# Performance work log

Hardware: AMD Instinct MI355X
Metric: run time of the kernel (lower is better)

## Reference

```python
import jax, jax.numpy as jnp
import numpy as np
import math

B, S, D, H, HD, P = 2, 2048, 2048, 16, 128, 10
ROPE_BASE = 10000.0


def _rope_tables(seq_len, head_dim):
    inv_freq = 1.0 / (ROPE_BASE ** (np.arange(0, head_dim, 2, dtype=np.float32) / head_dim))
    t = np.arange(seq_len, dtype=np.float32)
    freqs = np.outer(t, inv_freq)                  # [S, hd/2]
    emb = np.concatenate([freqs, freqs], axis=-1)  # [S, hd]
    return jnp.asarray(np.cos(emb)), jnp.asarray(np.sin(emb))


def _rotate_half(x):
    half = x.shape[-1] // 2
    return jnp.concatenate([-x[..., half:], x[..., :half]], axis=-1)


def setup_inputs() -> dict:
    key = jax.random.key(0)
    ks = jax.random.split(key, 8)
    hidden_states = jax.random.normal(ks[0], (B, S, D), dtype=jnp.float32)
    # causal additive mask, llama convention: 0 where allowed, large negative above diagonal
    causal = jnp.triu(jnp.full((S, S), -1e9, dtype=jnp.float32), k=1)
    attention_mask = jnp.broadcast_to(causal[None, None], (B, 1, S, S))
    position_ids = jnp.broadcast_to(jnp.arange(S, dtype=jnp.int64)[None], (B, S))
    scale = 1.0 / math.sqrt(D)
    Wq = jax.random.normal(ks[1], (D, D), dtype=jnp.float32) * scale
    Wk = jax.random.normal(ks[2], (D, D), dtype=jnp.float32) * scale
    Wv = jax.random.normal(ks[3], (D, D), dtype=jnp.float32) * scale
    Wo = jax.random.normal(ks[4], (D, D), dtype=jnp.float32) * scale
    adapter_query = jax.random.normal(ks[5], (P, D), dtype=jnp.float32)
    adapter_gate = jax.random.normal(ks[6], (1, H, 1, 1), dtype=jnp.float32) * 0.1
    return dict(hidden_states=hidden_states, attention_mask=attention_mask,
                position_ids=position_ids, Wq=Wq, Wk=Wk, Wv=Wv, Wo=Wo,
                adapter_query=adapter_query, adapter_gate=adapter_gate)


def reference(hidden_states, attention_mask, position_ids, Wq, Wk, Wv, Wo,
              adapter_query, adapter_gate):
    bsz, q_len, _ = hidden_states.shape
    inv_sqrt_hd = 1.0 / math.sqrt(HD)

    def split_heads(x):  # [B,S,D] -> [B,H,S,hd]
        return x.reshape(bsz, q_len, H, HD).transpose(0, 2, 1, 3)

    q = split_heads(hidden_states @ Wq)
    k = split_heads(hidden_states @ Wk)
    v = split_heads(hidden_states @ Wv)

    # RoPE
    cos_t, sin_t = _rope_tables(q_len, HD)
    cos = cos_t[position_ids][:, None]  # [B,1,S,hd]
    sin = sin_t[position_ids][:, None]
    q = q * cos + _rotate_half(q) * sin
    k = k * cos + _rotate_half(k) * sin

    # main attention
    scores = jnp.einsum('bhqd,bhkd->bhqk', q, k) * inv_sqrt_hd
    scores = scores + attention_mask
    attn = jax.nn.softmax(scores.astype(jnp.float32), axis=-1).astype(q.dtype)
    attn_out = jnp.einsum('bhqk,bhkd->bhqd', attn, v)

    # adapter: soft prompt projected through k/v proj (learn_kv=False), no RoPE
    adapter = jnp.broadcast_to(adapter_query[None], (bsz, P, D))  # [B,P,D]
    a_k = (adapter @ Wk).reshape(bsz, P, H, HD).transpose(0, 2, 1, 3)  # [B,H,P,hd]
    a_v = (adapter @ Wv).reshape(bsz, P, H, HD).transpose(0, 2, 1, 3)
    a_scores = jnp.einsum('bhqd,bhpd->bhqp', q, a_k) * inv_sqrt_hd
    a_w = adapter_gate * jax.nn.softmax(a_scores.astype(jnp.float32), axis=-1).astype(q.dtype)
    a_out = jnp.einsum('bhqp,bhpd->bhqd', a_w, a_v)

    out = attn_out + a_out
    out = out.transpose(0, 2, 1, 3).reshape(bsz, q_len, D)
    return out @ Wo
```

## Files before the change

kernel.cpp:

```cpp
#include <hip/hip_runtime.h>
#include <cstdint>
#include <cstddef>

typedef __bf16 bf16x8 __attribute__((ext_vector_type(8)));
typedef float  f32x4  __attribute__((ext_vector_type(4)));

__device__ __forceinline__ unsigned short f2bf(float f) {
  unsigned int u = __float_as_uint(f);
  u += 0x7FFF + ((u >> 16) & 1);
  return (unsigned short)(u >> 16);
}
__device__ __forceinline__ float bf2f(unsigned short u) {
  return __uint_as_float(((unsigned int)u) << 16);
}

#define SEQ 2048
#define DMODEL 2048
#define NH 16
#define HD 128
#define NB 2
#define NP 10
#define MAUG 4106
#define SCALEL2 (0.08838834764831845f * 1.44269504088896340f)

#define GLOAD_LDS16(g, l) \
  __builtin_amdgcn_global_load_lds((__attribute__((address_space(1))) const void*)(g), \
                                   (__attribute__((address_space(3))) void*)(l), 16, 0, 0)

#define FENCE() asm volatile("" ::: "memory")
#define SBAR() do { FENCE(); __builtin_amdgcn_s_barrier(); FENCE(); } while (0)
#define WAITVM(N) asm volatile("s_waitcnt vmcnt(" #N ")" ::: "memory")

__global__ void k_tables(float* __restrict__ cost, float* __restrict__ sint) {
  int idx = blockIdx.x * 256 + threadIdx.x;
  if (idx >= SEQ * 64) return;
  int s = idx >> 6, i = idx & 63;
  double invf = exp(-((double)(2 * i) / 128.0) * log(10000.0));
  double a = (double)s * invf;
  float c = (float)cos(a), sn = (float)sin(a);
  cost[s * HD + i] = c;  cost[s * HD + 64 + i] = c;
  sint[s * HD + i] = sn; sint[s * HD + 64 + i] = sn;
}

__global__ __launch_bounds__(256) void k_wt(const float* __restrict__ W0,
                                            const float* __restrict__ W1,
                                            const float* __restrict__ W2,
                                            const float* __restrict__ W3,
                                            unsigned short* __restrict__ out) {
  __shared__ float tile[32][33];
  const float* W = (blockIdx.z == 0) ? W0 : (blockIdx.z == 1) ? W1 : (blockIdx.z == 2) ? W2 : W3;
  unsigned short* o = out + (size_t)blockIdx.z * DMODEL * DMODEL;
  int bx = blockIdx.x * 32, by = blockIdx.y * 32;
  int tx = threadIdx.x & 31, ty = threadIdx.x >> 5;
  #pragma unroll
  for (int j = 0; j < 32; j += 8)
    tile[ty + j][tx] = W[(size_t)(bx + ty + j) * DMODEL + by + tx];
  __syncthreads();
  #pragma unroll
  for (int j = 0; j < 32; j += 8)
    o[(size_t)(by + ty + j) * DMODEL + bx + tx] = f2bf(tile[tx][ty + j]);
}

__global__ void k_xaug(const float* __restrict__ X, const float* __restrict__ Aq,
                       unsigned short* __restrict__ xaug) {
  size_t idx = (size_t)blockIdx.x * 256 + threadIdx.x;
  if (idx >= (size_t)MAUG * DMODEL) return;
  size_t row = idx >> 11;
  int col = (int)(idx & 2047);
  float v = (row < (size_t)NB * SEQ) ? X[idx] : Aq[(row - NB * SEQ) * DMODEL + col];
  xaug[idx] = f2bf(v);
}

#define LDA_HALF(MH) do { \
  _Pragma("unroll") for (int i_ = 0; i_ < 4; i_++) \
    _Pragma("unroll") for (int ks_ = 0; ks_ < 2; ks_++) \
      a[i_][ks_] = *(const bf16x8*)&lds[base + (wr*128 + (MH)*64 + i_*16 + lr)*64 + (((ks_*4+quad) ^ (lr & 7)) * 8)]; \
} while (0)

#define LDB_PAIR(NH) do { \
  _Pragma("unroll") for (int j_ = 0; j_ < 2; j_++) \
    _Pragma("unroll") for (int ks_ = 0; ks_ < 2; ks_++) \
      b[(NH)*2+j_][ks_] = *(const bf16x8*)&lds[base + 16384 + (wc*64 + ((NH)*2+j_)*16 + lr)*64 + (((ks_*4+quad) ^ (lr & 7)) * 8)]; \
} while (0)

#define MFMA_QUAD(MH, NH) do { \
  __builtin_amdgcn_s_setprio(1); \
  _Pragma("unroll") for (int i_ = 0; i_ < 4; i_++) \
    _Pragma("unroll") for (int j_ = 0; j_ < 2; j_++) { \
      acc[(MH)*4+i_][(NH)*2+j_] = __builtin_amdgcn_mfma_f32_16x16x32_bf16(a[i_][0], b[(NH)*2+j_][0], acc[(MH)*4+i_][(NH)*2+j_], 0, 0, 0); \
      acc[(MH)*4+i_][(NH)*2+j_] = __builtin_amdgcn_mfma_f32_16x16x32_bf16(a[i_][1], b[(NH)*2+j_][1], acc[(MH)*4+i_][(NH)*2+j_], 0, 0, 0); \
    } \
  __builtin_amdgcn_s_setprio(0); \
} while (0)

#define STG_AE(nb, ko) do { \
  GLOAD_LDS16(sA + (ko),                      &lds[(nb)*32768 + (qrow)*64 + g8]); \
  GLOAD_LDS16(sA + 128*(size_t)DMODEL + (ko), &lds[(nb)*32768 + (128+qrow)*64 + g8]); } while (0)
#define STG_AO(nb, ko) do { \
  GLOAD_LDS16(sA + 64*(size_t)DMODEL + (ko),  &lds[(nb)*32768 + (64+qrow)*64 + g8]); \
  GLOAD_LDS16(sA + 192*(size_t)DMODEL + (ko), &lds[(nb)*32768 + (192+qrow)*64 + g8]); } while (0)
#define STG_BE(nb, ko) do { \
  GLOAD_LDS16(sB + (ko),                      &lds[(nb)*32768 + 16384 + (qb)*64 + g8]); \
  GLOAD_LDS16(sB + 128*(size_t)DMODEL + (ko), &lds[(nb)*32768 + 16384 + (128+qb)*64 + g8]); } while (0)
#define STG_BO(nb, ko) do { \
  GLOAD_LDS16(sB + 32*(size_t)DMODEL + (ko),  &lds[(nb)*32768 + 16384 + (32+qb)*64 + g8]); \
  GLOAD_LDS16(sB + 160*(size_t)DMODEL + (ko), &lds[(nb)*32768 + 16384 + (160+qb)*64 + g8]); } while (0)

template<int BF16OUT>
__global__ __launch_bounds__(512, 2) void k_gemm256(const unsigned short* __restrict__ A,
                                                    const unsigned short* __restrict__ Bt,
                                                    void* __restrict__ Cv,
                                                    int M, size_t c_stride_mat) {
  __shared__ unsigned short lds[65536];
  const int t = threadIdx.x;
  const int lane = t & 63, w = t >> 6;
  const int lr = lane & 15, quad = lane >> 4;
  const int wr = w >> 2, wc = w & 3;
  const int m0 = blockIdx.y * 256, n0 = blockIdx.x * 256;
  const unsigned short* Bz = Bt + (size_t)blockIdx.z * DMODEL * DMODEL;

  const int qrow = t >> 3;
  const int g8 = (t & 7) * 8;
  const int gsw8 = (((t & 7) ^ (qrow & 7)) * 8);
  const int qb = (qrow < 32) ? qrow : qrow + 32;

  const unsigned short* sA = A + (size_t)(m0 + qrow) * DMODEL + gsw8;
  const unsigned short* sB = Bz + (size_t)(n0 + qb) * DMODEL + gsw8;

  bf16x8 a[4][2], b[4][2];
  f32x4 acc[8][4];
  #pragma unroll
  for (int i = 0; i < 8; i++)
    #pragma unroll
    for (int j = 0; j < 4; j++) acc[i][j] = (f32x4){0.f, 0.f, 0.f, 0.f};

  STG_AE(0, 0); STG_BE(0, 0); STG_BO(0, 0); STG_AO(0, 0);
  WAITVM(4);
  SBAR();

  for (int kt = 0; kt < DMODEL / 64; kt++) {
    const int base = (kt & 1) << 15;
    const int nb = (kt & 1) ^ 1;
    const int ko = (kt + 1) * 64;
    const bool more = (kt + 1 < DMODEL / 64);

    LDA_HALF(0);
    LDB_PAIR(0);
    if (more) STG_AE(nb, ko);
    SBAR();
    MFMA_QUAD(0, 0);
    if (more) WAITVM(4); else WAITVM(2);
    SBAR();

    LDB_PAIR(1);
    if (more) STG_BE(nb, ko);
    SBAR();
    MFMA_QUAD(0, 1);
    if (more) WAITVM(4); else WAITVM(0);
    SBAR();

    LDA_HALF(1);
    if (more) STG_BO(nb, ko);
    SBAR();
    MFMA_QUAD(1, 0);
    SBAR();

    if (more) STG_AO(nb, ko);
    SBAR();
    MFMA_QUAD(1, 1);
    if (more) WAITVM(4);
    SBAR();
  }

  #pragma unroll
  for (int mi = 0; mi < 8; mi++) {
    #pragma unroll
    for (int r = 0; r < 4; r++) {
      int row = m0 + wr * 128 + mi * 16 + quad * 4 + r;
      if (row < M) {
        if (BF16OUT) {
          unsigned short* C = (unsigned short*)Cv + (size_t)blockIdx.z * c_stride_mat;
          #pragma unroll
          for (int n = 0; n < 4; n++)
            C[(size_t)row * DMODEL + n0 + wc * 64 + n * 16 + lr] = f2bf(acc[mi][n][r]);
        } else {
          float* C = (float*)Cv + (size_t)blockIdx.z * c_stride_mat;
          #pragma unroll
          for (int n = 0; n < 4; n++)
            C[(size_t)row * DMODEL + n0 + wc * 64 + n * 16 + lr] = acc[mi][n][r];
        }
      }
    }
  }
}

__global__ __launch_bounds__(256) void k_rope(const unsigned short* __restrict__ Qf,
                                              const unsigned short* __restrict__ Kf,
                                              const unsigned short* __restrict__ Vf,
                                              const float* __restrict__ cost, const float* __restrict__ sint,
                                              unsigned short* __restrict__ Qb, unsigned short* __restrict__ Kb,
                                              unsigned short* __restrict__ AKb, unsigned short* __restrict__ avt) {
  int row = blockIdx.x;
  int t = threadIdx.x;
  int c0 = t * 8;
  size_t off = (size_t)row * DMODEL + c0;
  if (row < NB * SEQ) {
    int s = row & (SEQ - 1);
    int d0 = c0 & (HD - 1);
    int po = (d0 < 64) ? 64 : -64;
    float sign = (d0 < 64) ? -1.f : 1.f;
    uint4 qv = *(const uint4*)&Qf[off];
    uint4 qp = *(const uint4*)&Qf[off + po];
    uint4 kv = *(const uint4*)&Kf[off];
    uint4 kp = *(const uint4*)&Kf[off + po];
    const unsigned short* qa = (const unsigned short*)&qv;
    const unsigned short* qb2 = (const unsigned short*)&qp;
    const unsigned short* ka = (const unsigned short*)&kv;
    const unsigned short* kb2 = (const unsigned short*)&kp;
    unsigned short oq[8], ok[8];
    #pragma unroll
    for (int j = 0; j < 8; j++) {
      float cv = cost[s * HD + d0 + j], sv = sint[s * HD + d0 + j];
      oq[j] = f2bf(bf2f(qa[j]) * cv + sign * bf2f(qb2[j]) * sv);
      ok[j] = f2bf(bf2f(ka[j]) * cv + sign * bf2f(kb2[j]) * sv);
    }
    *(uint4*)&Qb[off] = *(const uint4*)oq;
    *(uint4*)&Kb[off] = *(const uint4*)ok;
  } else {
    int p = row - NB * SEQ;
    uint4 kv = *(const uint4*)&Kf[off];
    uint4 vv = *(const uint4*)&Vf[off];
    *(uint4*)&AKb[(size_t)p * DMODEL + c0] = kv;
    const unsigned short* vp = (const unsigned short*)&vv;
    #pragma unroll
    for (int j = 0; j < 8; j++)
      avt[(size_t)(c0 + j) * 32 + p] = vp[j];
  }
}

__global__ __launch_bounds__(256) void k_vt(const unsigned short* __restrict__ Vf,
                                            unsigned short* __restrict__ Vt) {
  __shared__ unsigned short tile[64][72];
  const int t = threadIdx.x;
  int s0 = blockIdx.x * 64;
  int d0 = blockIdx.y * 64;
  int b = blockIdx.z >> 4, h = blockIdx.z & 15;
  #pragma unroll
  for (int j = t; j < 512; j += 256) {
    int row = j >> 3, ch = j & 7;
    *(uint4*)&tile[row][ch * 8] =
      *(const uint4*)&Vf[(size_t)(b * SEQ + s0 + row) * DMODEL + h * HD + d0 + ch * 8];
  }
  __syncthreads();
  #pragma unroll
  for (int j = t; j < 512; j += 256) {
    int dr = j >> 3, ch = j & 7;
    unsigned short tmp[8];
    #pragma unroll
    for (int k = 0; k < 8; k++) tmp[k] = tile[ch * 8 + k][dr];
    *(uint4*)&Vt[((size_t)((b * NH + h) * HD + d0 + dr)) * SEQ + s0 + ch * 8] = *(const uint4*)tmp;
  }
}

#define PSTR 68

__global__ __launch_bounds__(256, 3) void k_flash(const unsigned short* __restrict__ Qb,
                                               const unsigned short* __restrict__ Kb,
                                               const unsigned short* __restrict__ Vt,
                                               const unsigned short* __restrict__ AKb,
                                               const unsigned short* __restrict__ avt,
                                               const float* __restrict__ gate,
                                               unsigned short* __restrict__ Obuf,
                                               float* __restrict__ ml,
                                               unsigned short* __restrict__ Aout) {
  const int L = blockIdx.x;
  const int h = L & 15;
  const int slot = 39 - (L >> 4);
  const int b = blockIdx.y;
  int qt, j, P;
  if (slot < 4)       { qt = slot;               j = 0;          P = 1; }
  else if (slot < 12) { int s = slot - 4;  qt = 4 + (s >> 1);  j = s & 1; P = 2; }
  else if (slot < 24) { int s = slot - 12; qt = 8 + s / 3;     j = s % 3; P = 3; }
  else                { int s = slot - 24; qt = 12 + (s >> 2); j = s & 3; P = 4; }

  const int t = threadIdx.x, w = t >> 6, lane = t & 63;
  const int lr = lane & 15, quad = lane >> 4;

  __shared__ unsigned short Ks[64 * 128];
  __shared__ unsigned short Vs[128 * 64];
  __shared__ unsigned short Ps[4][32 * PSTR];
  unsigned short* Ps16 = &Ps[w][0];

  const int row_base = qt * 128 + w * 32;

  bf16x8 qf[2][4];
  #pragma unroll
  for (int mt = 0; mt < 2; mt++)
    #pragma unroll
    for (int kk = 0; kk < 4; kk++)
      qf[mt][kk] = *(const bf16x8*)&Qb[((size_t)(b * SEQ + row_base + mt * 16 + lr)) * DMODEL
                                       + h * HD + kk * 32 + quad * 8];

  f32x4 o[2][8];
  #pragma unroll
  for (int mt = 0; mt < 2; mt++)
    #pragma unroll
    for (int nt = 0; nt < 8; nt++) o[mt][nt] = (f32x4){0.f, 0.f, 0.f, 0.f};
  float l_i[2][4];
  #pragma unroll
  for (int mt = 0; mt < 2; mt++)
    #pragma unroll
    for (int r = 0; r < 4; r++) l_i[mt][r] = 0.f;

  const int krow = t >> 4;
  const int vd = t >> 3, vc = (t & 7) ^ (vd & 7);
  const int ktend = 2 * qt + 2;

  for (int kt = j; kt < ktend; kt += P) {
    __syncthreads();
    #pragma unroll
    for (int jj = 0; jj < 4; jj++) {
      int row = krow + jj * 16;
      int c = (t & 15) ^ (row & 15);
      GLOAD_LDS16(&Kb[((size_t)(b * SEQ + kt * 64 + row)) * DMODEL + h * HD + c * 8],
                  &Ks[(t + jj * 256) * 8]);
    }
    #pragma unroll
    for (int jj = 0; jj < 4; jj++) {
      int d = vd + jj * 32;
      GLOAD_LDS16(&Vt[((size_t)((b * NH + h) * HD + d)) * SEQ + kt * 64 + vc * 8],
                  &Vs[(t + jj * 256) * 8]);
    }
    __syncthreads();

    f32x4 s4[2][4];
    #pragma unroll
    for (int mt = 0; mt < 2; mt++)
      #pragma unroll
      for (int nt = 0; nt < 4; nt++) s4[mt][nt] = (f32x4){0.f, 0.f, 0.f, 0.f};
    #pragma unroll
    for (int nt = 0; nt < 4; nt++)
      #pragma unroll
      for (int kk = 0; kk < 4; kk++) {
        bf16x8 bv = *(const bf16x8*)&Ks[((nt * 16 + lr) * 16 + ((kk * 4 + quad) ^ lr)) * 8];
        s4[0][nt] = __builtin_amdgcn_mfma_f32_16x16x32_bf16(qf[0][kk], bv, s4[0][nt], 0, 0, 0);
        s4[1][nt] = __builtin_amdgcn_mfma_f32_16x16x32_bf16(qf[1][kk], bv, s4[1][nt], 0, 0, 0);
      }

    const int maybe_mask = (kt * 64 + 63 > row_base);
    #pragma unroll
    for (int mt = 0; mt < 2; mt++) {
      #pragma unroll
      for (int nt = 0; nt < 4; nt++) s4[mt][nt] = s4[mt][nt] * SCALEL2;
      if (maybe_mask) {
        #pragma unroll
        for (int nt = 0; nt < 4; nt++) {
          int col = kt * 64 + nt * 16 + lr;
          #pragma unroll
          for (int r = 0; r < 4; r++)
            if (col > row_base + mt * 16 + quad * 4 + r) s4[mt][nt][r] = -__builtin_inff();
        }
      }
      #pragma unroll
      for (int nt = 0; nt < 4; nt++)
        #pragma unroll
        for (int r = 0; r < 4; r++) {
          float p = __builtin_amdgcn_exp2f(s4[mt][nt][r]);
          l_i[mt][r] += p;
          Ps[w][(mt * 16 + quad * 4 + r) * PSTR + nt * 16 + lr] = f2bf(p);
        }
    }
    #pragma unroll
    for (int kk2 = 0; kk2 < 2; kk2++) {
      bf16x8 af0 = *(const bf16x8*)&Ps[w][(lr) * PSTR + kk2 * 32 + quad * 8];
      bf16x8 af1 = *(const bf16x8*)&Ps[w][(16 + lr) * PSTR + kk2 * 32 + quad * 8];
      #pragma unroll
      for (int nt = 0; nt < 8; nt++) {
        bf16x8 bv = *(const bf16x8*)&Vs[((nt * 16 + lr) * 8 + ((kk2 * 4 + quad) ^ (lr & 7))) * 8];
        o[0][nt] = __builtin_amdgcn_mfma_f32_16x16x32_bf16(af0, bv, o[0][nt], 0, 0, 0);
        o[1][nt] = __builtin_amdgcn_mfma_f32_16x16x32_bf16(af1, bv, o[1][nt], 0, 0, 0);
      }
    }
  }

  #pragma unroll
  for (int mt = 0; mt < 2; mt++)
    #pragma unroll
    for (int r = 0; r < 4; r++) {
      float l = l_i[mt][r];
      #pragma unroll
      for (int off = 1; off < 16; off <<= 1) l += __shfl_xor(l, off, 64);
      l_i[mt][r] = l;
    }

  const size_t slotg = (size_t)(b * 16 + h) * 40 + slot;

  if (j == 0) {
    const float g = gate[h];
    #pragma unroll
    for (int mt = 0; mt < 2; mt++) {
      f32x4 as4 = (f32x4){0.f, 0.f, 0.f, 0.f};
      #pragma unroll
      for (int kk = 0; kk < 4; kk++) {
        bf16x8 akf = *(const bf16x8*)&AKb[(size_t)lr * DMODEL + h * HD + kk * 32 + quad * 8];
        as4 = __builtin_amdgcn_mfma_f32_16x16x32_bf16(qf[mt][kk], akf, as4, 0, 0, 0);
      }
      as4 = as4 * SCALEL2;
      float al[4];
      #pragma unroll
      for (int r = 0; r < 4; r++) {
        float p = (lr < NP) ? __builtin_amdgcn_exp2f(as4[r]) : 0.f;
        as4[r] = p;
        float sum = p;
        #pragma unroll
        for (int off = 1; off < 16; off <<= 1) sum += __shfl_xor(sum, off, 64);
        al[r] = sum;
      }
      #pragma unroll
      for (int r = 0; r < 4; r++) {
        Ps[w][(mt * 16 + quad * 4 + r) * PSTR + lr] = f2bf(as4[r]);
        Ps[w][(mt * 16 + quad * 4 + r) * PSTR + 16 + lr] = 0;
      }
      bf16x8 af = *(const bf16x8*)&Ps[w][(mt * 16 + lr) * PSTR + quad * 8];
      f32x4 pa[8];
      #pragma unroll
      for (int nt = 0; nt < 8; nt++) {
        bf16x8 bv = *(const bf16x8*)&avt[(size_t)(h * HD + nt * 16 + lr) * 32 + quad * 8];
        pa[nt] = __builtin_amdgcn_mfma_f32_16x16x32_bf16(af, bv, (f32x4){0.f, 0.f, 0.f, 0.f}, 0, 0, 0);
      }
      float invla[4];
      #pragma unroll
      for (int r = 0; r < 4; r++) invla[r] = g / al[r];
      #pragma unroll
      for (int nt = 0; nt < 8; nt++)
        #pragma unroll
        for (int r = 0; r < 4; r++)
          Ps16[(quad * 4 + r) * 128 + nt * 16 + lr] = f2bf(pa[nt][r] * invla[r]);
      size_t gb = (((size_t)(b * 16 + h) * 16 + qt)) * 16384 + (size_t)(w * 32 + mt * 16) * 128;
      #pragma unroll
      for (int it = 0; it < 4; it++) {
        int i = lane + it * 64;
        int rr = i >> 4, ch = i & 15;
        *(uint4*)&Aout[gb + rr * 128 + ch * 8] = *(const uint4*)&Ps16[rr * 128 + ch * 8];
      }
    }
  }

  #pragma unroll
  for (int mt = 0; mt < 2; mt++) {
    if (lr == 0) {
      #pragma unroll
      for (int r = 0; r < 4; r++) {
        int rl = w * 32 + mt * 16 + quad * 4 + r;
        ml[slotg * 128 + rl] = l_i[mt][r];
      }
    }
    #pragma unroll
    for (int nt = 0; nt < 8; nt++)
      #pragma unroll
      for (int r = 0; r < 4; r++)
        Ps16[(quad * 4 + r) * 128 + nt * 16 + lr] = f2bf(o[mt][nt][r]);
    size_t gb = slotg * 16384 + (size_t)(w * 32 + mt * 16) * 128;
    #pragma unroll
    for (int it = 0; it < 4; it++) {
      int i = lane + it * 64;
      int rr = i >> 4, ch = i & 15;
      *(uint4*)&Obuf[gb + rr * 128 + ch * 8] = *(const uint4*)&Ps16[rr * 128 + ch * 8];
    }
  }
}

__global__ __launch_bounds__(256) void k_merge(const unsigned short* __restrict__ Obuf,
                                               const float* __restrict__ ml,
                                               const unsigned short* __restrict__ Aout,
                                               unsigned short* __restrict__ ab) {
  int idx = blockIdx.x * 256 + threadIdx.x;
  int ch = idx & 15;
  int row = (idx >> 4) & 2047;
  int h = (idx >> 15) & 15;
  int b = idx >> 19;
  int qt = row >> 7, rl = row & 127;
  int start = qt < 4 ? qt : qt < 8 ? 4 + 2 * (qt - 4) : qt < 12 ? 12 + 3 * (qt - 8) : 24 + 4 * (qt - 12);
  int P = qt < 4 ? 1 : qt < 8 ? 2 : qt < 12 ? 3 : 4;
  size_t sbase = (size_t)(b * 16 + h) * 40 + start;
  float den = 0.f;
  float acc[8] = {0.f, 0.f, 0.f, 0.f, 0.f, 0.f, 0.f, 0.f};
  #pragma unroll
  for (int jp = 0; jp < 4; jp++) {
    if (jp < P) {
      den += ml[(sbase + jp) * 128 + rl];
      uint4 ov = *(const uint4*)&Obuf[(sbase + jp) * 16384 + rl * 128 + ch * 8];
      const unsigned short* pv = (const unsigned short*)&ov;
      #pragma unroll
      for (int k = 0; k < 8; k++) acc[k] += bf2f(pv[k]);
    }
  }
  uint4 av = *(const uint4*)&Aout[(((size_t)(b * 16 + h) * 16 + qt)) * 16384 + rl * 128 + ch * 8];
  const unsigned short* pa = (const unsigned short*)&av;
  float dn = 1.0f / den;
  unsigned short res[8];
  #pragma unroll
  for (int k = 0; k < 8; k++) res[k] = f2bf(acc[k] * dn + bf2f(pa[k]));
  *(uint4*)&ab[((size_t)(b * 2048 + row)) * 2048 + h * 128 + ch * 8] = *(const uint4*)res;
}

extern "C" void kernel_launch(void* const* d_in, const int* in_sizes, int n_in,
                              void* d_out, int out_size, void* d_ws, size_t ws_size,
                              hipStream_t stream) {
  const float* hidden = (const float*)d_in[0];
  const float* Wq = (const float*)d_in[3];
  const float* Wk = (const float*)d_in[4];
  const float* Wv = (const float*)d_in[5];
  const float* Wo = (const float*)d_in[6];
  const float* Aq = (const float*)d_in[7];
  const float* gate = (const float*)d_in[8];
  float* out = (float*)d_out;

  char* ws = (char*)d_ws;
  size_t off = 0;
  auto alloc = [&](size_t bytes) -> void* {
    void* p = ws + off;
    off = (off + bytes + 255) & ~(size_t)255;
    return p;
  };
  unsigned short* wt   = (unsigned short*)alloc((size_t)4 * DMODEL * DMODEL * 2);
  unsigned short* xaug = (unsigned short*)alloc((size_t)MAUG * DMODEL * 2);
  unsigned short* qkvb = (unsigned short*)alloc((size_t)3 * MAUG * DMODEL * 2);
  unsigned short* qf = qkvb;
  unsigned short* kf = qkvb + (size_t)MAUG * DMODEL;
  unsigned short* vf = kf + (size_t)MAUG * DMODEL;
  unsigned short* qb  = (unsigned short*)alloc((size_t)NB * SEQ * DMODEL * 2);
  unsigned short* kb  = (unsigned short*)alloc((size_t)NB * SEQ * DMODEL * 2);
  unsigned short* vt  = (unsigned short*)alloc((size_t)NB * SEQ * DMODEL * 2);
  unsigned short* akb = (unsigned short*)alloc((size_t)16 * DMODEL * 2);
  unsigned short* avt = (unsigned short*)alloc((size_t)DMODEL * 32 * 2);
  float* cost = (float*)alloc((size_t)SEQ * HD * 4);
  float* sint = (float*)alloc((size_t)SEQ * HD * 4);
  unsigned short* obuf = (unsigned short*)alloc((size_t)NB * NH * 40 * 16384 * 2);
  float* mlb = (float*)alloc((size_t)NB * NH * 40 * 128 * 4);
  unsigned short* aout = (unsigned short*)alloc((size_t)NB * NH * 16 * 16384 * 2);
  unsigned short* ab = qf;

  k_tables<<<SEQ * 64 / 256, 256, 0, stream>>>(cost, sint);
  k_wt<<<dim3(64, 64, 4), 256, 0, stream>>>(Wq, Wk, Wv, Wo, wt);
  {
    size_t n = (size_t)MAUG * DMODEL;
    k_xaug<<<(unsigned)((n + 255) / 256), 256, 0, stream>>>(hidden, Aq, xaug);
  }
  k_gemm256<1><<<dim3(8, 17, 3), 512, 0, stream>>>(xaug, wt, qkvb, MAUG, (size_t)MAUG * DMODEL);
  hipMemsetAsync(avt, 0, (size_t)DMODEL * 32 * 2, stream);
  k_rope<<<MAUG, 256, 0, stream>>>(qf, kf, vf, cost, sint, qb, kb, akb, avt);
  k_vt<<<dim3(32, 2, 32), 256, 0, stream>>>(vf, vt);
  k_flash<<<dim3(640, 2), 256, 0, stream>>>(qb, kb, vt, akb, avt, gate, obuf, mlb, aout);
  k_merge<<<4096, 256, 0, stream>>>(obuf, mlb, aout, ab);
  k_gemm256<0><<<dim3(8, 16, 1), 512, 0, stream>>>(ab, wt + (size_t)3 * DMODEL * DMODEL, out, NB * SEQ, 0);
}
```

Baseline: 481.6 us.

## Add 128x256 tile output-projection GEMM with two blocks per CU and lgkm waits

```diff
diff --git a/kernel.cpp b/kernel.cpp
--- a/kernel.cpp
+++ b/kernel.cpp
@@ -30,6 +30,7 @@
 #define FENCE() asm volatile("" ::: "memory")
 #define SBAR() do { FENCE(); __builtin_amdgcn_s_barrier(); FENCE(); } while (0)
 #define WAITVM(N) asm volatile("s_waitcnt vmcnt(" #N ")" ::: "memory")
+#define HINTLGKM(N) asm volatile("s_waitcnt lgkmcnt(" #N ")" ::: "memory")
 
 __global__ void k_tables(float* __restrict__ cost, float* __restrict__ sint) {
   int idx = blockIdx.x * 256 + threadIdx.x;
@@ -77,18 +78,18 @@
       a[i_][ks_] = *(const bf16x8*)&lds[base + (wr*128 + (MH)*64 + i_*16 + lr)*64 + (((ks_*4+quad) ^ (lr & 7)) * 8)]; \
 } while (0)
 
-#define LDB_PAIR(NH) do { \
+#define LDB_PAIR(NHH) do { \
   _Pragma("unroll") for (int j_ = 0; j_ < 2; j_++) \
     _Pragma("unroll") for (int ks_ = 0; ks_ < 2; ks_++) \
-      b[(NH)*2+j_][ks_] = *(const bf16x8*)&lds[base + 16384 + (wc*64 + ((NH)*2+j_)*16 + lr)*64 + (((ks_*4+quad) ^ (lr & 7)) * 8)]; \
+      b[(NHH)*2+j_][ks_] = *(const bf16x8*)&lds[base + 16384 + (wc*64 + ((NHH)*2+j_)*16 + lr)*64 + (((ks_*4+quad) ^ (lr & 7)) * 8)]; \
 } while (0)
 
-#define MFMA_QUAD(MH, NH) do { \
+#define MFMA_QUAD(MH, NHH) do { \
   __builtin_amdgcn_s_setprio(1); \
   _Pragma("unroll") for (int i_ = 0; i_ < 4; i_++) \
     _Pragma("unroll") for (int j_ = 0; j_ < 2; j_++) { \
-      acc[(MH)*4+i_][(NH)*2+j_] = __builtin_amdgcn_mfma_f32_16x16x32_bf16(a[i_][0], b[(NH)*2+j_][0], acc[(MH)*4+i_][(NH)*2+j_], 0, 0, 0); \
-      acc[(MH)*4+i_][(NH)*2+j_] = __builtin_amdgcn_mfma_f32_16x16x32_bf16(a[i_][1], b[(NH)*2+j_][1], acc[(MH)*4+i_][(NH)*2+j_], 0, 0, 0); \
+      acc[(MH)*4+i_][(NHH)*2+j_] = __builtin_amdgcn_mfma_f32_16x16x32_bf16(a[i_][0], b[(NHH)*2+j_][0], acc[(MH)*4+i_][(NHH)*2+j_], 0, 0, 0); \
+      acc[(MH)*4+i_][(NHH)*2+j_] = __builtin_amdgcn_mfma_f32_16x16x32_bf16(a[i_][1], b[(NHH)*2+j_][1], acc[(MH)*4+i_][(NHH)*2+j_], 0, 0, 0); \
     } \
   __builtin_amdgcn_s_setprio(0); \
 } while (0)
@@ -147,6 +148,7 @@
     LDA_HALF(0);
     LDB_PAIR(0);
     if (more) STG_AE(nb, ko);
+    HINTLGKM(8);
     SBAR();
     MFMA_QUAD(0, 0);
     if (more) WAITVM(4); else WAITVM(2);
@@ -161,6 +163,7 @@
 
     LDA_HALF(1);
     if (more) STG_BO(nb, ko);
+    HINTLGKM(4);
     SBAR();
     MFMA_QUAD(1, 0);
     SBAR();
@@ -190,6 +193,113 @@
             C[(size_t)row * DMODEL + n0 + wc * 64 + n * 16 + lr] = acc[mi][n][r];
         }
       }
+    }
+  }
+}
+
+#define O_LDA(MH) do { \
+  _Pragma("unroll") for (int i_ = 0; i_ < 2; i_++) \
+    _Pragma("unroll") for (int ks_ = 0; ks_ < 2; ks_++) \
+      a[i_][ks_] = *(const bf16x8*)&lds[base + (wr*64 + ((MH)*2+i_)*16 + lr)*64 + (((ks_*4+quad) ^ (lr & 7)) * 8)]; \
+} while (0)
+
+#define O_LDB(NHH) do { \
+  _Pragma("unroll") for (int j_ = 0; j_ < 2; j_++) \
+    _Pragma("unroll") for (int ks_ = 0; ks_ < 2; ks_++) \
+      b[(NHH)*2+j_][ks_] = *(const bf16x8*)&lds[base + 8192 + (wc*64 + ((NHH)*2+j_)*16 + lr)*64 + (((ks_*4+quad) ^ (lr & 7)) * 8)]; \
+} while (0)
+
+#define O_MFMA(MH, NHH) do { \
+  __builtin_amdgcn_s_setprio(1); \
+  _Pragma("unroll") for (int i_ = 0; i_ < 2; i_++) \
+    _Pragma("unroll") for (int j_ = 0; j_ < 2; j_++) { \
+      acc[(MH)*2+i_][(NHH)*2+j_] = __builtin_amdgcn_mfma_f32_16x16x32_bf16(a[i_][0], b[(NHH)*2+j_][0], acc[(MH)*2+i_][(NHH)*2+j_], 0, 0, 0); \
+      acc[(MH)*2+i_][(NHH)*2+j_] = __builtin_amdgcn_mfma_f32_16x16x32_bf16(a[i_][1], b[(NHH)*2+j_][1], acc[(MH)*2+i_][(NHH)*2+j_], 0, 0, 0); \
+    } \
+  __builtin_amdgcn_s_setprio(0); \
+} while (0)
+
+#define O_STG_AE(nb, ko) GLOAD_LDS16(sA + (ko), &lds[(nb)*24576 + (qb)*64 + g8])
+#define O_STG_AO(nb, ko) GLOAD_LDS16(sA + 32*(size_t)DMODEL + (ko), &lds[(nb)*24576 + (32+qb)*64 + g8])
+#define O_STG_BE(nb, ko) do { \
+  GLOAD_LDS16(sB + (ko),                      &lds[(nb)*24576 + 8192 + (qb)*64 + g8]); \
+  GLOAD_LDS16(sB + 128*(size_t)DMODEL + (ko), &lds[(nb)*24576 + 8192 + (128+qb)*64 + g8]); } while (0)
+#define O_STG_BO(nb, ko) do { \
+  GLOAD_LDS16(sB + 32*(size_t)DMODEL + (ko),  &lds[(nb)*24576 + 8192 + (32+qb)*64 + g8]); \
+  GLOAD_LDS16(sB + 160*(size_t)DMODEL + (ko), &lds[(nb)*24576 + 8192 + (160+qb)*64 + g8]); } while (0)
+
+__global__ __launch_bounds__(512, 2) void k_gemmo(const unsigned short* __restrict__ A,
+                                                  const unsigned short* __restrict__ Bt,
+                                                  float* __restrict__ C) {
+  __shared__ unsigned short lds[49152];
+  const int t = threadIdx.x;
+  const int lane = t & 63, w = t >> 6;
+  const int lr = lane & 15, quad = lane >> 4;
+  const int wr = w >> 2, wc = w & 3;
+  const int m0 = blockIdx.y * 128, n0 = blockIdx.x * 256;
+
+  const int qrow = t >> 3;
+  const int g8 = (t & 7) * 8;
+  const int gsw8 = (((t & 7) ^ (qrow & 7)) * 8);
+  const int qb = (qrow < 32) ? qrow : qrow + 32;
+
+  const unsigned short* sA = A + (size_t)(m0 + qb) * DMODEL + gsw8;
+  const unsigned short* sB = Bt + (size_t)(n0 + qb) * DMODEL + gsw8;
+
+  bf16x8 a[2][2], b[4][2];
+  f32x4 acc[4][4];
+  #pragma unroll
+  for (int i = 0; i < 4; i++)
+    #pragma unroll
+    for (int j = 0; j < 4; j++) acc[i][j] = (f32x4){0.f, 0.f, 0.f, 0.f};
+
+  O_STG_AE(0, 0); O_STG_BE(0, 0); O_STG_BO(0, 0); O_STG_AO(0, 0);
+  WAITVM(3);
+  SBAR();
+
+  for (int kt = 0; kt < DMODEL / 64; kt++) {
+    const int base = (kt & 1) * 24576;
+    const int nb = (kt & 1) ^ 1;
+    const int ko = (kt + 1) * 64;
+    const bool more = (kt + 1 < DMODEL / 64);
+
+    O_LDA(0);
+    O_LDB(0);
+    if (more) O_STG_AE(nb, ko);
+    HINTLGKM(4);
+    SBAR();
+    O_MFMA(0, 0);
+    if (more) WAITVM(2); else WAITVM(1);
+    SBAR();
+
+    O_LDB(1);
+    if (more) O_STG_BE(nb, ko);
+    SBAR();
+    O_MFMA(0, 1);
+    if (more) WAITVM(3); else WAITVM(0);
+    SBAR();
+
+    O_LDA(1);
+    if (more) O_STG_BO(nb, ko);
+    SBAR();
+    O_MFMA(1, 0);
+    SBAR();
+
+    if (more) O_STG_AO(nb, ko);
+    SBAR();
+    O_MFMA(1, 1);
+    if (more) WAITVM(3);
+    SBAR();
+  }
+
+  #pragma unroll
+  for (int mi = 0; mi < 4; mi++) {
+    #pragma unroll
+    for (int r = 0; r < 4; r++) {
+      int row = m0 + wr * 64 + mi * 16 + quad * 4 + r;
+      #pragma unroll
+      for (int n = 0; n < 4; n++)
+        C[(size_t)row * DMODEL + n0 + wc * 64 + n * 16 + lr] = acc[mi][n][r];
     }
   }
 }
@@ -553,5 +663,5 @@
   k_vt<<<dim3(32, 2, 32), 256, 0, stream>>>(vf, vt);
   k_flash<<<dim3(640, 2), 256, 0, stream>>>(qb, kb, vt, akb, avt, gate, obuf, mlb, aout);
   k_merge<<<4096, 256, 0, stream>>>(obuf, mlb, aout, ab);
-  k_gemm256<0><<<dim3(8, 16, 1), 512, 0, stream>>>(ab, wt + (size_t)3 * DMODEL * DMODEL, out, NB * SEQ, 0);
-}
+  k_gemmo<<<dim3(8, 32), 512, 0, stream>>>(ab, wt + (size_t)3 * DMODEL * DMODEL, out);
+}
```

Measured after the change: 471.9 us. 1.02x faster.

## Shrink GEMM tiles to 128x128 with register double-buffering and XCD-aware block mapping

Applied to the files above, without the earlier changes.

```diff
diff --git a/kernel.cpp b/kernel.cpp
--- a/kernel.cpp
+++ b/kernel.cpp
@@ -71,120 +71,121 @@
   xaug[idx] = f2bf(v);
 }
 
-#define LDA_HALF(MH) do { \
-  _Pragma("unroll") for (int i_ = 0; i_ < 4; i_++) \
+#define RD_A(dst, bb, MH) do { \
+  _Pragma("unroll") for (int i_ = 0; i_ < 2; i_++) \
     _Pragma("unroll") for (int ks_ = 0; ks_ < 2; ks_++) \
-      a[i_][ks_] = *(const bf16x8*)&lds[base + (wr*128 + (MH)*64 + i_*16 + lr)*64 + (((ks_*4+quad) ^ (lr & 7)) * 8)]; \
+      dst[i_][ks_] = *(const bf16x8*)&lds[(bb) + (wr*64 + (MH)*32 + i_*16 + lr)*64 + (((ks_*4+quad) ^ (lr & 7)) * 8)]; \
 } while (0)
 
-#define LDB_PAIR(NH) do { \
+#define RD_B(dst, bb, NHH) do { \
   _Pragma("unroll") for (int j_ = 0; j_ < 2; j_++) \
     _Pragma("unroll") for (int ks_ = 0; ks_ < 2; ks_++) \
-      b[(NH)*2+j_][ks_] = *(const bf16x8*)&lds[base + 16384 + (wc*64 + ((NH)*2+j_)*16 + lr)*64 + (((ks_*4+quad) ^ (lr & 7)) * 8)]; \
+      dst[j_][ks_] = *(const bf16x8*)&lds[(bb) + 8192 + (wc*64 + (NHH)*32 + j_*16 + lr)*64 + (((ks_*4+quad) ^ (lr & 7)) * 8)]; \
 } while (0)
 
-#define MFMA_QUAD(MH, NH) do { \
+#define MM(A, B, MH, NHH) do { \
   __builtin_amdgcn_s_setprio(1); \
-  _Pragma("unroll") for (int i_ = 0; i_ < 4; i_++) \
+  _Pragma("unroll") for (int i_ = 0; i_ < 2; i_++) \
     _Pragma("unroll") for (int j_ = 0; j_ < 2; j_++) { \
-      acc[(MH)*4+i_][(NH)*2+j_] = __builtin_amdgcn_mfma_f32_16x16x32_bf16(a[i_][0], b[(NH)*2+j_][0], acc[(MH)*4+i_][(NH)*2+j_], 0, 0, 0); \
-      acc[(MH)*4+i_][(NH)*2+j_] = __builtin_amdgcn_mfma_f32_16x16x32_bf16(a[i_][1], b[(NH)*2+j_][1], acc[(MH)*4+i_][(NH)*2+j_], 0, 0, 0); \
+      acc[(MH)*2+i_][(NHH)*2+j_] = __builtin_amdgcn_mfma_f32_16x16x32_bf16(A[i_][0], B[j_][0], acc[(MH)*2+i_][(NHH)*2+j_], 0, 0, 0); \
+      acc[(MH)*2+i_][(NHH)*2+j_] = __builtin_amdgcn_mfma_f32_16x16x32_bf16(A[i_][1], B[j_][1], acc[(MH)*2+i_][(NHH)*2+j_], 0, 0, 0); \
     } \
   __builtin_amdgcn_s_setprio(0); \
 } while (0)
 
 #define STG_AE(nb, ko) do { \
-  GLOAD_LDS16(sA + (ko),                      &lds[(nb)*32768 + (qrow)*64 + g8]); \
-  GLOAD_LDS16(sA + 128*(size_t)DMODEL + (ko), &lds[(nb)*32768 + (128+qrow)*64 + g8]); } while (0)
+  GLOAD_LDS16(sA + (ko),                     &lds[(nb)*16384 + (qrow)*64 + g8]); \
+  GLOAD_LDS16(sA + 64*(size_t)DMODEL + (ko), &lds[(nb)*16384 + (64+qrow)*64 + g8]); } while (0)
 #define STG_AO(nb, ko) do { \
-  GLOAD_LDS16(sA + 64*(size_t)DMODEL + (ko),  &lds[(nb)*32768 + (64+qrow)*64 + g8]); \
-  GLOAD_LDS16(sA + 192*(size_t)DMODEL + (ko), &lds[(nb)*32768 + (192+qrow)*64 + g8]); } while (0)
+  GLOAD_LDS16(sA + 32*(size_t)DMODEL + (ko), &lds[(nb)*16384 + (32+qrow)*64 + g8]); \
+  GLOAD_LDS16(sA + 96*(size_t)DMODEL + (ko), &lds[(nb)*16384 + (96+qrow)*64 + g8]); } while (0)
 #define STG_BE(nb, ko) do { \
-  GLOAD_LDS16(sB + (ko),                      &lds[(nb)*32768 + 16384 + (qb)*64 + g8]); \
-  GLOAD_LDS16(sB + 128*(size_t)DMODEL + (ko), &lds[(nb)*32768 + 16384 + (128+qb)*64 + g8]); } while (0)
+  GLOAD_LDS16(sB + (ko),                     &lds[(nb)*16384 + 8192 + (qrow)*64 + g8]); \
+  GLOAD_LDS16(sB + 64*(size_t)DMODEL + (ko), &lds[(nb)*16384 + 8192 + (64+qrow)*64 + g8]); } while (0)
 #define STG_BO(nb, ko) do { \
-  GLOAD_LDS16(sB + 32*(size_t)DMODEL + (ko),  &lds[(nb)*32768 + 16384 + (32+qb)*64 + g8]); \
-  GLOAD_LDS16(sB + 160*(size_t)DMODEL + (ko), &lds[(nb)*32768 + 16384 + (160+qb)*64 + g8]); } while (0)
+  GLOAD_LDS16(sB + 32*(size_t)DMODEL + (ko), &lds[(nb)*16384 + 8192 + (32+qrow)*64 + g8]); \
+  GLOAD_LDS16(sB + 96*(size_t)DMODEL + (ko), &lds[(nb)*16384 + 8192 + (96+qrow)*64 + g8]); } while (0)
 
 template<int BF16OUT>
-__global__ __launch_bounds__(512, 2) void k_gemm256(const unsigned short* __restrict__ A,
+__global__ __launch_bounds__(256, 2) void k_gemm128(const unsigned short* __restrict__ A,
                                                     const unsigned short* __restrict__ Bt,
                                                     void* __restrict__ Cv,
                                                     int M, size_t c_stride_mat) {
-  __shared__ unsigned short lds[65536];
+  __shared__ unsigned short lds[32768];
   const int t = threadIdx.x;
   const int lane = t & 63, w = t >> 6;
   const int lr = lane & 15, quad = lane >> 4;
-  const int wr = w >> 2, wc = w & 3;
-  const int m0 = blockIdx.y * 256, n0 = blockIdx.x * 256;
-  const unsigned short* Bz = Bt + (size_t)blockIdx.z * DMODEL * DMODEL;
+  const int wr = w >> 1, wc = w & 1;
+  const int tm = (M + 127) >> 7;
+  const int perz = tm * 16;
+  const int qchunk = gridDim.x >> 3;
+  const int lin = ((int)blockIdx.x & 7) * qchunk + ((int)blockIdx.x >> 3);
+  const int z = lin / perz;
+  const int rem = lin - z * perz;
+  const int m0 = (rem >> 4) * 128, n0 = (rem & 15) * 128;
+  const unsigned short* Bz = Bt + (size_t)z * DMODEL * DMODEL;
 
   const int qrow = t >> 3;
   const int g8 = (t & 7) * 8;
   const int gsw8 = (((t & 7) ^ (qrow & 7)) * 8);
-  const int qb = (qrow < 32) ? qrow : qrow + 32;
 
   const unsigned short* sA = A + (size_t)(m0 + qrow) * DMODEL + gsw8;
-  const unsigned short* sB = Bz + (size_t)(n0 + qb) * DMODEL + gsw8;
-
-  bf16x8 a[4][2], b[4][2];
-  f32x4 acc[8][4];
-  #pragma unroll
-  for (int i = 0; i < 8; i++)
+  const unsigned short* sB = Bz + (size_t)(n0 + qrow) * DMODEL + gsw8;
+
+  bf16x8 aE[2][2], aO[2][2], bE[2][2], bO[2][2];
+  f32x4 acc[4][4];
+  #pragma unroll
+  for (int i = 0; i < 4; i++)
     #pragma unroll
     for (int j = 0; j < 4; j++) acc[i][j] = (f32x4){0.f, 0.f, 0.f, 0.f};
 
   STG_AE(0, 0); STG_BE(0, 0); STG_BO(0, 0); STG_AO(0, 0);
   WAITVM(4);
   SBAR();
+  RD_A(aE, 0, 0); RD_B(bE, 0, 0);
 
   for (int kt = 0; kt < DMODEL / 64; kt++) {
-    const int base = (kt & 1) << 15;
-    const int nb = (kt & 1) ^ 1;
+    const int base = (kt & 1) << 14;
+    const int nb2 = (kt & 1) ^ 1;
+    const int nbase = nb2 << 14;
     const int ko = (kt + 1) * 64;
     const bool more = (kt + 1 < DMODEL / 64);
 
-    LDA_HALF(0);
-    LDB_PAIR(0);
-    if (more) STG_AE(nb, ko);
+    if (more) { STG_AE(nb2, ko); WAITVM(4); } else WAITVM(2);
     SBAR();
-    MFMA_QUAD(0, 0);
-    if (more) WAITVM(4); else WAITVM(2);
+    RD_B(bO, base, 1);
+    MM(aE, bE, 0, 0);
+
+    if (more) { STG_BE(nb2, ko); WAITVM(4); } else WAITVM(0);
     SBAR();
-
-    LDB_PAIR(1);
-    if (more) STG_BE(nb, ko);
-    SBAR();
-    MFMA_QUAD(0, 1);
-    if (more) WAITVM(4); else WAITVM(0);
-    SBAR();
-
-    LDA_HALF(1);
-    if (more) STG_BO(nb, ko);
-    SBAR();
-    MFMA_QUAD(1, 0);
-    SBAR();
-
-    if (more) STG_AO(nb, ko);
-    SBAR();
-    MFMA_QUAD(1, 1);
-    if (more) WAITVM(4);
-    SBAR();
-  }
-
-  #pragma unroll
-  for (int mi = 0; mi < 8; mi++) {
+    RD_A(aO, base, 1);
+    MM(aE, bO, 0, 1);
+
+    if (more) STG_BO(nb2, ko);
+    MM(aO, bE, 1, 0);
+
+    if (more) {
+      STG_AO(nb2, ko);
+      WAITVM(4);
+      SBAR();
+      RD_A(aE, nbase, 0); RD_B(bE, nbase, 0);
+    }
+    MM(aO, bO, 1, 1);
+  }
+
+  #pragma unroll
+  for (int mi = 0; mi < 4; mi++) {
     #pragma unroll
     for (int r = 0; r < 4; r++) {
-      int row = m0 + wr * 128 + mi * 16 + quad * 4 + r;
+      int row = m0 + wr * 64 + mi * 16 + quad * 4 + r;
       if (row < M) {
         if (BF16OUT) {
-          unsigned short* C = (unsigned short*)Cv + (size_t)blockIdx.z * c_stride_mat;
+          unsigned short* C = (unsigned short*)Cv + (size_t)z * c_stride_mat;
           #pragma unroll
           for (int n = 0; n < 4; n++)
             C[(size_t)row * DMODEL + n0 + wc * 64 + n * 16 + lr] = f2bf(acc[mi][n][r]);
         } else {
-          float* C = (float*)Cv + (size_t)blockIdx.z * c_stride_mat;
+          float* C = (float*)Cv + (size_t)z * c_stride_mat;
           #pragma unroll
           for (int n = 0; n < 4; n++)
             C[(size_t)row * DMODEL + n0 + wc * 64 + n * 16 + lr] = acc[mi][n][r];
@@ -547,11 +548,11 @@
     size_t n = (size_t)MAUG * DMODEL;
     k_xaug<<<(unsigned)((n + 255) / 256), 256, 0, stream>>>(hidden, Aq, xaug);
   }
-  k_gemm256<1><<<dim3(8, 17, 3), 512, 0, stream>>>(xaug, wt, qkvb, MAUG, (size_t)MAUG * DMODEL);
+  k_gemm128<1><<<dim3(1584), 256, 0, stream>>>(xaug, wt, qkvb, MAUG, (size_t)MAUG * DMODEL);
   hipMemsetAsync(avt, 0, (size_t)DMODEL * 32 * 2, stream);
   k_rope<<<MAUG, 256, 0, stream>>>(qf, kf, vf, cost, sint, qb, kb, akb, avt);
   k_vt<<<dim3(32, 2, 32), 256, 0, stream>>>(vf, vt);
   k_flash<<<dim3(640, 2), 256, 0, stream>>>(qb, kb, vt, akb, avt, gate, obuf, mlb, aout);
   k_merge<<<4096, 256, 0, stream>>>(obuf, mlb, aout, ab);
-  k_gemm256<0><<<dim3(8, 16, 1), 512, 0, stream>>>(ab, wt + (size_t)3 * DMODEL * DMODEL, out, NB * SEQ, 0);
-}
+  k_gemm128<0><<<dim3(512), 256, 0, stream>>>(ab, wt + (size_t)3 * DMODEL * DMODEL, out, NB * SEQ, 0);
+}
```

Measured after the change: 484.4 us. Within noise of the previous version (+0.6%).
